# Kernel optimization log

Hardware: AMD Instinct MI355X
Metric: run time of the kernel (lower is better)

The kernel has to match this reference:

```python
import jax, jax.numpy as jnp
import numpy as np

N = 40000            # atoms
ER = 2_500_000       # radial edges
EA = 1_200_000       # angular edges
P = 4_000_000        # angle triples
NUM_SPECIES = 4      # H,C,N,O
CUTOFF = 5.2
ANG_CUTOFF = 3.5
RADIAL_ETA = 16.0
ANGULAR_ETA = 8.0
RDIV = 16
ADIV = 4
ZETA = 32.0
ASEC = 4
RSTART = 0.8
ASTART = 0.8


def setup_inputs() -> dict:
    key = jax.random.key(0)
    ks = jax.random.split(key, 12)
    species = jax.random.randint(ks[0], (N,), 0, NUM_SPECIES, dtype=jnp.int32)
    rad_distances = jax.random.uniform(ks[1], (ER,), jnp.float32, RSTART, CUTOFF)
    rad_switch = jax.random.uniform(ks[2], (ER,), jnp.float32)
    edge_src = jax.random.randint(ks[3], (ER,), 0, N, dtype=jnp.int32)
    edge_dst = jax.random.randint(ks[4], (ER,), 0, N, dtype=jnp.int32)
    ang_distances = jax.random.uniform(ks[5], (EA,), jnp.float32, ASTART, ANG_CUTOFF)
    ang_switch = jax.random.uniform(ks[6], (EA,), jnp.float32)
    angles = jax.random.uniform(ks[7], (P,), jnp.float32, 0.0, float(np.pi))
    central_atom = jax.random.randint(ks[8], (P,), 0, N, dtype=jnp.int32)
    angle_src = jax.random.randint(ks[9], (P,), 0, EA, dtype=jnp.int32)
    angle_dst = jax.random.randint(ks[10], (P,), 0, EA, dtype=jnp.int32)
    ang_edge_dst = jax.random.randint(ks[11], (EA,), 0, N, dtype=jnp.int32)
    return {
        "species": species,
        "rad_distances": rad_distances,
        "rad_switch": rad_switch,
        "edge_src": edge_src,
        "edge_dst": edge_dst,
        "ang_distances": ang_distances,
        "ang_switch": ang_switch,
        "angles": angles,
        "central_atom": central_atom,
        "angle_src": angle_src,
        "angle_dst": angle_dst,
        "ang_edge_dst": ang_edge_dst,
    }


def _triu_table(nsp):
    s1, s2 = np.triu_indices(nsp, 0)
    t = np.zeros((nsp, nsp), dtype=np.int32)
    t[s1, s2] = np.arange(s1.shape[0], dtype=np.int32)
    t[s2, s1] = t[s1, s2]
    return jnp.asarray(t)


def reference(species, rad_distances, rad_switch, edge_src, edge_dst,
              ang_distances, ang_switch, angles, central_atom,
              angle_src, angle_dst, ang_edge_dst):
    n_atoms = species.shape[0]
    nsp = NUM_SPECIES
    nsp_pair = nsp * (nsp + 1) // 2
    indices = species  # already species-order indices in [0, nsp)

    # ---- radial AEV ----
    shiftR = jnp.asarray(-np.linspace(RSTART, CUTOFF, RDIV + 1)[None, :-1],
                         dtype=rad_distances.dtype)  # [1, RDIV]
    x2 = RADIAL_ETA * (rad_distances[:, None] + shiftR) ** 2       # [ER, RDIV]
    radial_terms = jnp.exp(-x2) * (0.25 * rad_switch)[:, None]
    radial_index = edge_src * nsp + indices[edge_dst]
    radial_aev = jax.ops.segment_sum(radial_terms, radial_index,
                                     num_segments=nsp * n_atoms)
    radial_aev = radial_aev.reshape(n_atoms, nsp * RDIV)

    # ---- angular AEV ----
    dist = 0.5 * ANGULAR_ETA ** 0.5 * ang_distances                # [EA]
    d12 = (dist[angle_src] + dist[angle_dst])[:, None]             # [P, 1]
    angle_start = np.pi / (2 * ASEC)
    shiftZ = jnp.asarray(-(np.linspace(0, np.pi, ASEC + 1) + angle_start)[None, :-1],
                         dtype=dist.dtype)                          # [1, ASEC]
    shiftA = jnp.asarray(-ANGULAR_ETA ** 0.5 *
                         np.linspace(ASTART, ANG_CUTOFF, ADIV + 1)[None, :-1],
                         dtype=dist.dtype)                          # [1, ADIV]
    sw = ang_switch * (2.0 * 0.5 ** ZETA) ** 0.5                   # [EA]
    f1 = sw[angle_src] * sw[angle_dst]                             # [P]
    factor1 = f1[:, None] * (1 + jnp.cos(angles[:, None] + shiftZ)) ** ZETA  # [P, ASEC]
    factor2 = jnp.exp(-(d12 + shiftA) ** 2)                        # [P, ADIV]
    angular_terms = (factor1[:, None, :] * factor2[:, :, None]).reshape(-1, ASEC * ADIV)

    idx_dest = indices[ang_edge_dst]                               # [EA]
    triu = _triu_table(nsp)
    angular_index = central_atom * nsp_pair + triu[idx_dest[angle_src], idx_dest[angle_dst]]
    angular_aev = jax.ops.segment_sum(angular_terms, angular_index,
                                      num_segments=nsp_pair * n_atoms)
    angular_aev = angular_aev.reshape(n_atoms, nsp_pair * ASEC * ADIV)

    return jnp.concatenate((radial_aev, angular_aev), axis=-1)     # [N, 224]
```

## Files before the change

### kernel.cpp

```cpp
#include <hip/hip_runtime.h>


constexpr int kOutCols  = 224;
constexpr int kAngBase  = 64;
constexpr int kABUCK    = 64;
constexpr int kMaxBins  = 640;
constexpr int kSCap     = 4096;
constexpr int kNBR      = 640;
constexpr int kNBA      = 1024;
constexpr int kRCap     = 4608;
constexpr int kACap     = 7168;
constexpr int kRC       = 12;
constexpr int kCapR     = 16;
constexpr int kCapA     = 12;
constexpr int kOvf      = 512;

__device__ __constant__ int c_triu[16] = {0,1,2,3, 1,4,5,6, 2,5,7,8, 3,6,8,9};
__device__ __constant__ float c_ca[4] = {0.92387953f, 0.38268343f, -0.38268343f, -0.92387953f};
__device__ __constant__ float c_sa[4] = {0.38268343f, 0.92387953f,  0.92387953f,  0.38268343f};
__device__ __constant__ float c_sh[4] = {-2.2627417f, -4.1719303f, -6.0811183f, -7.9903066f};

constexpr float kThQ  = 20860.437f;
constexpr float kRevD = 7.6295109e-6f;
constexpr float kD12B = 2.2627417f;
constexpr float kD12S = 1.4974026e-2f;
constexpr float kF1D  = 1.1732081e-13f;
constexpr float kRdS  = 930.6818f;
constexpr float kRdD  = 1.0744811e-3f;
constexpr float kRswD = 6.1050061e-5f;

__device__ __forceinline__ int scan1024_exc(int cv, int tid, int* wsum, int* total)
{
    int lane = tid & 63, wv = tid >> 6;
    int x = cv;
    #pragma unroll
    for (int o = 1; o < 64; o <<= 1) {
        int t = __shfl_up(x, o, 64);
        if (lane >= o) x += t;
    }
    if (lane == 63) wsum[wv] = x;
    __syncthreads();
    if (wv == 0 && lane < 16) {
        int s = wsum[lane];
        #pragma unroll
        for (int o = 1; o < 16; o <<= 1) {
            int t = __shfl_up(s, o, 64);
            if (lane >= o) s += t;
        }
        wsum[lane] = s;
    }
    __syncthreads();
    int base = (wv == 0) ? 0 : wsum[wv - 1];
    *total = wsum[15];
    return base + x - cv;
}

__global__ void prep(const float* __restrict__ ang_d, const float* __restrict__ ang_sw,
                     const int* __restrict__ aed, const int* __restrict__ species,
                     unsigned short* __restrict__ eaq, int EA)
{
    int i = blockIdx.x * blockDim.x + threadIdx.x;
    if (i >= EA) return;
    float dq = fmaxf(ang_d[i] - 0.8f, 0.0f) * (255.0f / 2.7f);
    unsigned qd = min((unsigned)(dq + 0.5f), 255u);
    unsigned qs = min((unsigned)(fmaxf(ang_sw[i], 0.0f) * 63.0f + 0.5f), 63u);
    unsigned sp = (unsigned)species[aed[i]];
    eaq[i] = (unsigned short)(qd | (qs << 8) | (sp << 14));
}

__global__ __launch_bounds__(1024)
void scat(const float* __restrict__ rd, const float* __restrict__ rsw,
          const int* __restrict__ esrc, const int* __restrict__ edst,
          const int* __restrict__ species,
          unsigned* __restrict__ rrec, int* __restrict__ offRT, int ER, int chR,
          const float* __restrict__ angles, const int* __restrict__ cat,
          const int* __restrict__ asrc, const int* __restrict__ adst,
          const unsigned short* __restrict__ eaq,
          uint2* __restrict__ arec, int* __restrict__ offAT, int P, int chA)
{
    __shared__ uint2 sbuf[kMaxBins * kCapA];
    __shared__ int cur[kMaxBins], off[kMaxBins + 1];
    __shared__ int wsum[16];
    __shared__ int ovfn;
    __shared__ uint4 ovfb[kOvf];
    int tid = threadIdx.x;

    if (blockIdx.x < kNBR) {
        unsigned* stage = (unsigned*)sbuf;
        for (int t = tid; t < kMaxBins; t += 1024) cur[t] = t * kCapR;
        if (tid == 0) ovfn = 0;
        __syncthreads();
        int sb  = blockIdx.x;
        int beg = sb * chR, end = min(beg + chR, ER);
        int i0 = beg + tid * 4;
        if (i0 < end) {
            float4 d4 = *reinterpret_cast<const float4*>(rd + i0);
            float4 s4 = *reinterpret_cast<const float4*>(rsw + i0);
            int4   e4 = *reinterpret_cast<const int4*>(esrc + i0);
            int4   t4 = *reinterpret_cast<const int4*>(edst + i0);
            unsigned sa = (unsigned)species[t4.x], sb2 = (unsigned)species[t4.y];
            unsigned sc2 = (unsigned)species[t4.z], sd = (unsigned)species[t4.w];
            auto bld = [](float d, float s, int e, unsigned sp, unsigned& v, int& k) {
                unsigned qd = min((unsigned)(fmaxf(d - 0.8f, 0.0f) * kRdS + 0.5f), 4095u);
                unsigned qs = min((unsigned)(fmaxf(s, 0.0f) * 4095.0f + 0.5f), 4095u);
                v = qd | (qs << 12) | (sp << 24) | ((unsigned)(e & 63) << 26);
                k = e >> 6;
            };
            unsigned v0, v1, v2, v3; int k0, k1, k2, k3;
            bld(d4.x, s4.x, e4.x, sa,  v0, k0);
            bld(d4.y, s4.y, e4.y, sb2, v1, k1);
            bld(d4.z, s4.z, e4.z, sc2, v2, k2);
            bld(d4.w, s4.w, e4.w, sd,  v3, k3);
            auto ins = [&](int k, unsigned v) {
                int pos = atomicAdd(&cur[k], 1);
                int loc = pos - k * kCapR;
                if (loc < kCapR) stage[pos] = v;
                else {
                    int o = atomicAdd(&ovfn, 1);
                    if (o < kOvf) { ovfb[o].x = (unsigned)k; ovfb[o].y = (unsigned)loc; ovfb[o].z = v; }
                }
            };
            ins(k0, v0); ins(k1, v1); ins(k2, v2); ins(k3, v3);
        }
        __syncthreads();
        int cv = (tid < kMaxBins) ? (cur[tid] - tid * kCapR) : 0;
        int tot;
        int exc = scan1024_exc(cv, tid, wsum, &tot);
        if (tid < kMaxBins) off[tid] = exc;
        if (tid == 0) off[kMaxBins] = tot;
        if (tid < kMaxBins) cur[tid] = min(cv, kCapR);
        __syncthreads();
        for (int s = tid; s < kMaxBins * kCapR; s += 1024) {
            int bin = s >> 4, loc = s & (kCapR - 1);
            if (loc < cur[bin]) rrec[beg + off[bin] + loc] = stage[s];
        }
        int no = min(ovfn, kOvf);
        for (int o = tid; o < no; o += 1024) {
            uint4 e = ovfb[o];
            rrec[beg + off[e.x] + (int)e.y] = e.z;
        }
        for (int t = tid; t <= kMaxBins; t += 1024) offRT[t * kNBR + sb] = off[t];
    } else {
        for (int t = tid; t < kMaxBins; t += 1024) cur[t] = t * kCapA;
        if (tid == 0) ovfn = 0;
        __syncthreads();
        int sb  = blockIdx.x - kNBR;
        int beg = sb * chA, end = min(beg + chA, P);
        int i0 = beg + tid * 4;
        if (i0 < end) {
            uint4  s4 = *reinterpret_cast<const uint4*>(asrc + i0);
            uint4  d4 = *reinterpret_cast<const uint4*>(adst + i0);
            float4 t4 = *reinterpret_cast<const float4*>(angles + i0);
            int4   c4 = *reinterpret_cast<const int4*>(cat + i0);
            unsigned qa0 = eaq[s4.x], qb0 = eaq[d4.x];
            unsigned qa1 = eaq[s4.y], qb1 = eaq[d4.y];
            unsigned qa2 = eaq[s4.z], qb2 = eaq[d4.z];
            unsigned qa3 = eaq[s4.w], qb3 = eaq[d4.w];
            auto bld = [](unsigned qa, unsigned qb, float th, int atom, uint2& rv, int& key) {
                unsigned qd12 = (qa & 255u) + (qb & 255u);
                unsigned qf1  = ((qa >> 8) & 63u) * ((qb >> 8) & 63u);
                int pair = c_triu[(qa >> 14) * 4 + (qb >> 14)];
                unsigned qt = min((unsigned)(fmaxf(th, 0.0f) * kThQ + 0.5f), 65535u);
                rv.x = qt | (qd12 << 16);
                rv.y = qf1 | ((unsigned)((atom & 63) * 10 + pair) << 16);
                key = atom >> 6;
            };
            uint2 r0, r1, r2, r3; int k0, k1, k2, k3;
            bld(qa0, qb0, t4.x, c4.x, r0, k0);
            bld(qa1, qb1, t4.y, c4.y, r1, k1);
            bld(qa2, qb2, t4.z, c4.z, r2, k2);
            bld(qa3, qb3, t4.w, c4.w, r3, k3);
            auto ins = [&](int k, uint2 r) {
                int pos = atomicAdd(&cur[k], 1);
                int loc = pos - k * kCapA;
                if (loc < kCapA) sbuf[pos] = r;
                else {
                    int o = atomicAdd(&ovfn, 1);
                    if (o < kOvf) { ovfb[o].x = (unsigned)k; ovfb[o].y = (unsigned)loc; ovfb[o].z = r.x; ovfb[o].w = r.y; }
                }
            };
            ins(k0, r0); ins(k1, r1); ins(k2, r2); ins(k3, r3);
        }
        __syncthreads();
        int cv = (tid < kMaxBins) ? (cur[tid] - tid * kCapA) : 0;
        int tot;
        int exc = scan1024_exc(cv, tid, wsum, &tot);
        if (tid < kMaxBins) off[tid] = exc;
        if (tid == 0) off[kMaxBins] = tot;
        if (tid < kMaxBins) cur[tid] = min(cv, kCapA);
        __syncthreads();
        for (int s = tid; s < kMaxBins * kCapA; s += 1024) {
            int bin = s / kCapA, loc = s - bin * kCapA;
            if (loc < cur[bin]) arec[beg + off[bin] + loc] = sbuf[s];
        }
        int no = min(ovfn, kOvf);
        for (int o = tid; o < no; o += 1024) {
            uint4 e = ovfb[o];
            uint2 r; r.x = e.z; r.y = e.w;
            arec[beg + off[e.x] + (int)e.y] = r;
        }
        for (int t = tid; t <= kMaxBins; t += 1024) offAT[t * kNBA + sb] = off[t];
    }
}

__global__ __launch_bounds__(1024)
void acc_rad(const unsigned* __restrict__ rrec, const int* __restrict__ offRT,
             int chR, float* __restrict__ out, int N)
{
    __shared__ unsigned rb[kRCap];
    __shared__ int cnt[64], off[65], cur[64];
    int b = blockIdx.x, tid = threadIdx.x;
    int gstart = 0, glen = 0;
    if (tid < kNBR) {
        int s0 = offRT[b * kNBR + tid];
        int s1 = offRT[(b + 1) * kNBR + tid];
        gstart = tid * chR + s0;
        glen   = s1 - s0;
    }
    unsigned rr[kRC];
    int gl = min(glen, kRC);
    #pragma unroll
    for (int q = 0; q < kRC; ++q) if (q < gl) rr[q] = rrec[gstart + q];
    if (tid < 64) cnt[tid] = 0;
    __syncthreads();
    #pragma unroll
    for (int q = 0; q < kRC; ++q) if (q < gl) atomicAdd(&cnt[(rr[q] >> 26) & 63], 1);
    for (int p = gstart + kRC; p < gstart + glen; ++p)
        atomicAdd(&cnt[(rrec[p] >> 26) & 63], 1);
    __syncthreads();
    if (tid < 64) {
        int x = cnt[tid], v = x;
        #pragma unroll
        for (int o = 1; o < 64; o <<= 1) {
            int t = __shfl_up(v, o, 64);
            if (tid >= o) v += t;
        }
        off[tid] = v - x; cur[tid] = v - x;
        if (tid == 63) off[64] = v;
    }
    __syncthreads();
    #pragma unroll
    for (int q = 0; q < kRC; ++q)
        if (q < gl) {
            int pos = atomicAdd(&cur[(rr[q] >> 26) & 63], 1);
            if (pos < kRCap) rb[pos] = rr[q];
        }
    for (int p = gstart + kRC; p < gstart + glen; ++p) {
        unsigned r = rrec[p];
        int pos = atomicAdd(&cur[(r >> 26) & 63], 1);
        if (pos < kRCap) rb[pos] = r;
    }
    __syncthreads();
    int lane = tid & 63, wave = tid >> 6;
    int q = lane >> 4, k = lane & 15;
    float ck = fmaf(0.275f, (float)k, 0.8f);
    for (int row = wave; row < kABUCK; row += 16) {
        int s  = min(off[row], kRCap);
        int e1 = min(off[row + 1], kRCap);
        float a0 = 0, a1 = 0, a2 = 0, a3 = 0;
        for (int p = s + q; p < e1; p += 4) {
            unsigned r = rb[p];
            float d  = fmaf((float)(r & 4095u), kRdD, 0.8f);
            float sw = (float)((r >> 12) & 4095u) * kRswD;
            int sp   = (r >> 24) & 3;
            float x  = d - ck;
            float v  = sw * __expf(-16.0f * x * x);
            a0 += (sp == 0) ? v : 0.0f;
            a1 += (sp == 1) ? v : 0.0f;
            a2 += (sp == 2) ? v : 0.0f;
            a3 += (sp == 3) ? v : 0.0f;
        }
        a0 += __shfl_xor(a0, 16, 64); a0 += __shfl_xor(a0, 32, 64);
        a1 += __shfl_xor(a1, 16, 64); a1 += __shfl_xor(a1, 32, 64);
        a2 += __shfl_xor(a2, 16, 64); a2 += __shfl_xor(a2, 32, 64);
        a3 += __shfl_xor(a3, 16, 64); a3 += __shfl_xor(a3, 32, 64);
        float val = (q == 0) ? a0 : (q == 1) ? a1 : (q == 2) ? a2 : a3;
        int atom = b * kABUCK + row;
        if (atom < N) out[(size_t)atom * kOutCols + lane] = val;
    }
}

__global__ __launch_bounds__(1024)
void acc_ang(const uint2* __restrict__ arec, const int* __restrict__ offAT,
             int chA, float* __restrict__ out, int N)
{
    __shared__ uint2 ab[kACap];
    __shared__ int cnt[640], off[641], cur[640];
    __shared__ int wsum[16];
    int b = blockIdx.x, tid = threadIdx.x;
    int s0 = offAT[b * kNBA + tid];
    int s1 = offAT[(b + 1) * kNBA + tid];
    int gstart = tid * chA + s0;
    int glen   = s1 - s0;
    uint2 rr[kRC];
    int gl = min(glen, kRC);
    #pragma unroll
    for (int q = 0; q < kRC; ++q) if (q < gl) rr[q] = arec[gstart + q];
    for (int t = tid; t < 640; t += 1024) cnt[t] = 0;
    __syncthreads();
    #pragma unroll
    for (int q = 0; q < kRC; ++q) if (q < gl) atomicAdd(&cnt[rr[q].y >> 16], 1);
    for (int p = gstart + kRC; p < gstart + glen; ++p)
        atomicAdd(&cnt[arec[p].y >> 16], 1);
    __syncthreads();
    int cv = (tid < 640) ? cnt[tid] : 0;
    int tot;
    int exc = scan1024_exc(cv, tid, wsum, &tot);
    if (tid < 640) { off[tid] = exc; cur[tid] = exc; }
    if (tid == 0) off[640] = tot;
    __syncthreads();
    #pragma unroll
    for (int q = 0; q < kRC; ++q)
        if (q < gl) {
            int pos = atomicAdd(&cur[rr[q].y >> 16], 1);
            if (pos < kACap) ab[pos] = rr[q];
        }
    for (int p = gstart + kRC; p < gstart + glen; ++p) {
        uint2 r = arec[p];
        int pos = atomicAdd(&cur[r.y >> 16], 1);
        if (pos < kACap) ab[pos] = r;
    }
    __syncthreads();
    int g = tid >> 4, lam = tid & 15;
    int q = lam >> 2, j = lam & 3;
    float caj = c_ca[j], saj = c_sa[j];
    int atom = b * kABUCK + g;
    if (atom < N) {
        float* orow = out + (size_t)atom * kOutCols + kAngBase;
        for (int pr = 0; pr < 10; ++pr) {
            int s  = min(off[g * 10 + pr], kACap);
            int e1 = min(off[g * 10 + pr + 1], kACap);
            float s0v = 0, s1v = 0, s2v = 0, s3v = 0;
            for (int p = s + q; p < e1; p += 4) {
                uint2 r = ab[p];
                float rev = (float)(r.x & 0xFFFFu) * kRevD;
                float d12 = fmaf((float)(r.x >> 16), kD12S, kD12B);
                float f1  = (float)(r.y & 0xFFFFu) * kF1D;
                float sn, cs;
                asm("v_sin_f32 %0, %1" : "=v"(sn) : "v"(rev));
                asm("v_cos_f32 %0, %1" : "=v"(cs) : "v"(rev));
                float cj = fmaf(cs, caj, sn * saj);
                float t  = 1.0f + cj;
                float t2 = t * t, t4 = t2 * t2, t8 = t4 * t4, t16 = t8 * t8;
                float w  = f1 * (t16 * t16);
                float x0 = d12 + c_sh[0]; s0v = fmaf(w, __expf(-x0 * x0), s0v);
                float x1 = d12 + c_sh[1]; s1v = fmaf(w, __expf(-x1 * x1), s1v);
                float x2 = d12 + c_sh[2]; s2v = fmaf(w, __expf(-x2 * x2), s2v);
                float x3 = d12 + c_sh[3]; s3v = fmaf(w, __expf(-x3 * x3), s3v);
            }
            s0v += __shfl_xor(s0v, 4, 64); s0v += __shfl_xor(s0v, 8, 64);
            s1v += __shfl_xor(s1v, 4, 64); s1v += __shfl_xor(s1v, 8, 64);
            s2v += __shfl_xor(s2v, 4, 64); s2v += __shfl_xor(s2v, 8, 64);
            s3v += __shfl_xor(s3v, 4, 64); s3v += __shfl_xor(s3v, 8, 64);
            float val = (q == 0) ? s0v : (q == 1) ? s1v : (q == 2) ? s2v : s3v;
            orow[pr * 16 + lam] = val;
        }
    }
}

__global__ void radial_kernel(const float* __restrict__ rd, const float* __restrict__ rsw,
                              const int* __restrict__ esrc, const int* __restrict__ edst,
                              const int* __restrict__ species,
                              float* __restrict__ out, int ER)
{
    int i = blockIdx.x * blockDim.x + threadIdx.x;
    if (i >= ER) return;
    float d   = rd[i];
    float sw  = 0.25f * rsw[i];
    int   src = esrc[i];
    int   sp  = species[edst[i]];
    float* base = out + (size_t)src * kOutCols + sp * 16;
    float t = (d - 0.8f) * (1.0f / 0.275f);
    int klo = max(0, (int)ceilf(t - 4.0f));
    int khi = min(15, (int)floorf(t + 4.0f));
    for (int k = klo; k <= khi; ++k) {
        float x = d - fmaf(0.275f, (float)k, 0.8f);
        float v = sw * __expf(-16.0f * x * x);
        if (v > 1e-8f) unsafeAtomicAdd(base + k, v);
    }
}

__global__ void angular_fallback(const float* __restrict__ angles, const int* __restrict__ cat,
                                 const int* __restrict__ asrc, const int* __restrict__ adst,
                                 const float* __restrict__ ang_d, const float* __restrict__ ang_sw,
                                 const int* __restrict__ aed, const int* __restrict__ species,
                                 float* __restrict__ out, int P)
{
    int i = blockIdx.x * blockDim.x + threadIdx.x;
    if (i >= P) return;
    int e1i = asrc[i], e2i = adst[i];
    float d1 = 1.41421356237f * ang_d[e1i];
    float d2 = 1.41421356237f * ang_d[e2i];
    float w1 = 2.1579187e-05f * ang_sw[e1i];
    float w2 = 2.1579187e-05f * ang_sw[e2i];
    int sp1 = species[aed[e1i]], sp2 = species[aed[e2i]];
    float d12 = d1 + d2;
    float f1  = w1 * w2;
    int pair = c_triu[sp1 * 4 + sp2];
    float* base = out + (size_t)cat[i] * kOutCols + kAngBase + pair * 16;

    float s, c;
    __sincosf(angles[i], &s, &c);
    const float ca0 = 0.92387953f, sa0 = 0.38268343f;
    float cth[4];
    cth[0] = fmaf(c,  ca0, s * sa0);
    cth[1] = fmaf(c,  sa0, s * ca0);
    cth[2] = fmaf(c, -sa0, s * ca0);
    cth[3] = fmaf(c, -ca0, s * sa0);
    float fac1[4];
    #pragma unroll
    for (int j = 0; j < 4; ++j) {
        float t  = 1.0f + cth[j];
        float t2 = t * t, t4 = t2 * t2, t8 = t4 * t4, t16 = t8 * t8;
        fac1[j]  = f1 * (t16 * t16);
    }
    const float shiftA[4] = {-2.2627417f, -4.1719303f, -6.0811183f, -7.9903066f};
    #pragma unroll
    for (int ii = 0; ii < 4; ++ii) {
        float x  = d12 + shiftA[ii];
        float f2 = __expf(-x * x);
        if (f2 < 1e-7f) continue;
        #pragma unroll
        for (int j = 0; j < 4; ++j) {
            float v = f2 * fac1[j];
            if (v > 1e-8f) unsafeAtomicAdd(base + ii * 4 + j, v);
        }
    }
}

extern "C" void kernel_launch(void* const* d_in, const int* in_sizes, int n_in,
                              void* d_out, int out_size, void* d_ws, size_t ws_size,
                              hipStream_t stream)
{
    const int*   species = (const int*)  d_in[0];
    const float* rad_d   = (const float*)d_in[1];
    const float* rad_sw  = (const float*)d_in[2];
    const int*   esrc    = (const int*)  d_in[3];
    const int*   edst    = (const int*)  d_in[4];
    const float* ang_d   = (const float*)d_in[5];
    const float* ang_sw  = (const float*)d_in[6];
    const float* angles  = (const float*)d_in[7];
    const int*   cat     = (const int*)  d_in[8];
    const int*   asrc    = (const int*)  d_in[9];
    const int*   adst    = (const int*)  d_in[10];
    const int*   aed     = (const int*)  d_in[11];
    float* out = (float*)d_out;

    const int N  = in_sizes[0];
    const int ER = in_sizes[1];
    const int EA = in_sizes[5];
    const int P  = in_sizes[7];

    const int NB  = (N + kABUCK - 1) / kABUCK;
    const int chR = (((ER + kNBR - 1) / kNBR) + 3) & ~3;
    const int chA = (((P  + kNBA - 1) / kNBA) + 3) & ~3;

    char* w = (char*)d_ws;
    size_t pos = 0;
    auto take = [&](size_t nbytes) {
        size_t cur = pos;
        pos = (pos + nbytes + 255) & ~(size_t)255;
        return cur;
    };
    size_t ea_o   = take((size_t)EA * 2);
    size_t rrec_o = take((size_t)kNBR * chR * 4);
    size_t arec_o = take((size_t)kNBA * chA * 8);
    size_t ort_o  = take((size_t)(kMaxBins + 1) * kNBR * 4);
    size_t oat_o  = take((size_t)(kMaxBins + 1) * kNBA * 4);
    const size_t need = pos;

    const bool sorted_ok = (ws_size >= need) && (NB <= kMaxBins) &&
                           (chR <= kSCap) && (chA <= kSCap) &&
                           ((P & 3) == 0) && ((ER & 3) == 0);

    if (sorted_ok) {
        unsigned short* eaq = (unsigned short*)(w + ea_o);
        unsigned* rrec  = (unsigned*)(w + rrec_o);
        uint2*    arec  = (uint2*)(w + arec_o);
        int*      offRT = (int*)(w + ort_o);
        int*      offAT = (int*)(w + oat_o);

        prep<<<(EA + 255) / 256, 256, 0, stream>>>(ang_d, ang_sw, aed, species, eaq, EA);
        scat<<<kNBR + kNBA, 1024, 0, stream>>>(rad_d, rad_sw, esrc, edst, species,
                                               rrec, offRT, ER, chR,
                                               angles, cat, asrc, adst, eaq,
                                               arec, offAT, P, chA);
        acc_rad<<<NB, 1024, 0, stream>>>(rrec, offRT, chR, out, N);
        acc_ang<<<NB, 1024, 0, stream>>>(arec, offAT, chA, out, N);
    } else {
        hipMemsetAsync(d_out, 0, (size_t)out_size * sizeof(float), stream);
        radial_kernel<<<(ER + 255) / 256, 256, 0, stream>>>(rad_d, rad_sw, esrc, edst, species, out, ER);
        angular_fallback<<<(P + 255) / 256, 256, 0, stream>>>(angles, cat, asrc, adst,
                                                              ang_d, ang_sw, aed, species, out, P);
    }
}
```

Baseline: 178.7 us.

## Regroup stages into fused launches to overlap radial scatter with angular prep

Moves the angular-edge quantisation (prep) into the same launch as the radial scatter, and moves the radial accumulation into the same launch as the angular scatter, using block-index ranges to select each role. This cuts four launches to three and lets independent stages run side by side on the GPU, so idle tails between dependent kernels are reduced. Shared memory is now carved manually from one raw buffer per role. The fused1 kernel now needs only the radial staging buffer, which may lower its LDS footprint. The cost is that fused2 blocks reserve the larger angular LDS size even when doing radial accumulation, which may limit occupancy.

```diff
diff --git a/kernel.cpp b/kernel.cpp
--- a/kernel.cpp
+++ b/kernel.cpp
@@ -55,30 +55,15 @@
     return base + x - cv;
 }
 
-__global__ void prep(const float* __restrict__ ang_d, const float* __restrict__ ang_sw,
-                     const int* __restrict__ aed, const int* __restrict__ species,
-                     unsigned short* __restrict__ eaq, int EA)
-{
-    int i = blockIdx.x * blockDim.x + threadIdx.x;
-    if (i >= EA) return;
-    float dq = fmaxf(ang_d[i] - 0.8f, 0.0f) * (255.0f / 2.7f);
-    unsigned qd = min((unsigned)(dq + 0.5f), 255u);
-    unsigned qs = min((unsigned)(fmaxf(ang_sw[i], 0.0f) * 63.0f + 0.5f), 63u);
-    unsigned sp = (unsigned)species[aed[i]];
-    eaq[i] = (unsigned short)(qd | (qs << 8) | (sp << 14));
-}
-
 __global__ __launch_bounds__(1024)
-void scat(const float* __restrict__ rd, const float* __restrict__ rsw,
-          const int* __restrict__ esrc, const int* __restrict__ edst,
-          const int* __restrict__ species,
-          unsigned* __restrict__ rrec, int* __restrict__ offRT, int ER, int chR,
-          const float* __restrict__ angles, const int* __restrict__ cat,
-          const int* __restrict__ asrc, const int* __restrict__ adst,
-          const unsigned short* __restrict__ eaq,
-          uint2* __restrict__ arec, int* __restrict__ offAT, int P, int chA)
-{
-    __shared__ uint2 sbuf[kMaxBins * kCapA];
+void fused1(const float* __restrict__ rd, const float* __restrict__ rsw,
+            const int* __restrict__ esrc, const int* __restrict__ edst,
+            const int* __restrict__ species,
+            unsigned* __restrict__ rrec, int* __restrict__ offRT, int ER, int chR,
+            const float* __restrict__ ang_d, const float* __restrict__ ang_sw,
+            const int* __restrict__ aed, unsigned short* __restrict__ eaq, int EA)
+{
+    __shared__ unsigned stage[kMaxBins * kCapR];
     __shared__ int cur[kMaxBins], off[kMaxBins + 1];
     __shared__ int wsum[16];
     __shared__ int ovfn;
@@ -86,7 +71,6 @@
     int tid = threadIdx.x;
 
     if (blockIdx.x < kNBR) {
-        unsigned* stage = (unsigned*)sbuf;
         for (int t = tid; t < kMaxBins; t += 1024) cur[t] = t * kCapR;
         if (tid == 0) ovfn = 0;
         __syncthreads();
@@ -141,10 +125,40 @@
         }
         for (int t = tid; t <= kMaxBins; t += 1024) offRT[t * kNBR + sb] = off[t];
     } else {
+        int i = (blockIdx.x - kNBR) * 1024 + tid;
+        if (i < EA) {
+            float dq = fmaxf(ang_d[i] - 0.8f, 0.0f) * (255.0f / 2.7f);
+            unsigned qd = min((unsigned)(dq + 0.5f), 255u);
+            unsigned qs = min((unsigned)(fmaxf(ang_sw[i], 0.0f) * 63.0f + 0.5f), 63u);
+            unsigned sp = (unsigned)species[aed[i]];
+            eaq[i] = (unsigned short)(qd | (qs << 8) | (sp << 14));
+        }
+    }
+}
+
+__global__ __launch_bounds__(1024)
+void fused2(const float* __restrict__ angles, const int* __restrict__ cat,
+            const int* __restrict__ asrc, const int* __restrict__ adst,
+            const unsigned short* __restrict__ eaq,
+            uint2* __restrict__ arec, int* __restrict__ offAT, int P, int chA,
+            const unsigned* __restrict__ rrec, const int* __restrict__ offRT,
+            int chR, float* __restrict__ out, int N)
+{
+    __shared__ uint4 raw[4680];
+    int tid = threadIdx.x;
+
+    if (blockIdx.x < kNBA) {
+        uint2* sbuf = (uint2*)raw;
+        int*   cur  = (int*)((char*)raw + 61440);
+        int*   off  = (int*)((char*)raw + 64000);
+        int*   wsum = (int*)((char*)raw + 66564);
+        int*   ovfn = (int*)((char*)raw + 66628);
+        uint4* ovfb = (uint4*)((char*)raw + 66640);
+
         for (int t = tid; t < kMaxBins; t += 1024) cur[t] = t * kCapA;
-        if (tid == 0) ovfn = 0;
-        __syncthreads();
-        int sb  = blockIdx.x - kNBR;
+        if (tid == 0) *ovfn = 0;
+        __syncthreads();
+        int sb  = blockIdx.x;
         int beg = sb * chA, end = min(beg + chA, P);
         int i0 = beg + tid * 4;
         if (i0 < end) {
@@ -175,7 +189,7 @@
                 int loc = pos - k * kCapA;
                 if (loc < kCapA) sbuf[pos] = r;
                 else {
-                    int o = atomicAdd(&ovfn, 1);
+                    int o = atomicAdd(ovfn, 1);
                     if (o < kOvf) { ovfb[o].x = (unsigned)k; ovfb[o].y = (unsigned)loc; ovfb[o].z = r.x; ovfb[o].w = r.y; }
                 }
             };
@@ -193,90 +207,88 @@
             int bin = s / kCapA, loc = s - bin * kCapA;
             if (loc < cur[bin]) arec[beg + off[bin] + loc] = sbuf[s];
         }
-        int no = min(ovfn, kOvf);
+        int no = min(*ovfn, kOvf);
         for (int o = tid; o < no; o += 1024) {
             uint4 e = ovfb[o];
             uint2 r; r.x = e.z; r.y = e.w;
             arec[beg + off[e.x] + (int)e.y] = r;
         }
         for (int t = tid; t <= kMaxBins; t += 1024) offAT[t * kNBA + sb] = off[t];
-    }
-}
-
-__global__ __launch_bounds__(1024)
-void acc_rad(const unsigned* __restrict__ rrec, const int* __restrict__ offRT,
-             int chR, float* __restrict__ out, int N)
-{
-    __shared__ unsigned rb[kRCap];
-    __shared__ int cnt[64], off[65], cur[64];
-    int b = blockIdx.x, tid = threadIdx.x;
-    int gstart = 0, glen = 0;
-    if (tid < kNBR) {
-        int s0 = offRT[b * kNBR + tid];
-        int s1 = offRT[(b + 1) * kNBR + tid];
-        gstart = tid * chR + s0;
-        glen   = s1 - s0;
-    }
-    unsigned rr[kRC];
-    int gl = min(glen, kRC);
-    #pragma unroll
-    for (int q = 0; q < kRC; ++q) if (q < gl) rr[q] = rrec[gstart + q];
-    if (tid < 64) cnt[tid] = 0;
-    __syncthreads();
-    #pragma unroll
-    for (int q = 0; q < kRC; ++q) if (q < gl) atomicAdd(&cnt[(rr[q] >> 26) & 63], 1);
-    for (int p = gstart + kRC; p < gstart + glen; ++p)
-        atomicAdd(&cnt[(rrec[p] >> 26) & 63], 1);
-    __syncthreads();
-    if (tid < 64) {
-        int x = cnt[tid], v = x;
+    } else {
+        unsigned* rb  = (unsigned*)raw;
+        int*      cnt = (int*)((char*)raw + 18432);
+        int*      off = (int*)((char*)raw + 18688);
+        int*      cur = (int*)((char*)raw + 18948);
+
+        int b = blockIdx.x - kNBA;
+        int gstart = 0, glen = 0;
+        if (tid < kNBR) {
+            int s0 = offRT[b * kNBR + tid];
+            int s1 = offRT[(b + 1) * kNBR + tid];
+            gstart = tid * chR + s0;
+            glen   = s1 - s0;
+        }
+        unsigned rr[kRC];
+        int gl = min(glen, kRC);
         #pragma unroll
-        for (int o = 1; o < 64; o <<= 1) {
-            int t = __shfl_up(v, o, 64);
-            if (tid >= o) v += t;
-        }
-        off[tid] = v - x; cur[tid] = v - x;
-        if (tid == 63) off[64] = v;
-    }
-    __syncthreads();
-    #pragma unroll
-    for (int q = 0; q < kRC; ++q)
-        if (q < gl) {
-            int pos = atomicAdd(&cur[(rr[q] >> 26) & 63], 1);
-            if (pos < kRCap) rb[pos] = rr[q];
-        }
-    for (int p = gstart + kRC; p < gstart + glen; ++p) {
-        unsigned r = rrec[p];
-        int pos = atomicAdd(&cur[(r >> 26) & 63], 1);
-        if (pos < kRCap) rb[pos] = r;
-    }
-    __syncthreads();
-    int lane = tid & 63, wave = tid >> 6;
-    int q = lane >> 4, k = lane & 15;
-    float ck = fmaf(0.275f, (float)k, 0.8f);
-    for (int row = wave; row < kABUCK; row += 16) {
-        int s  = min(off[row], kRCap);
-        int e1 = min(off[row + 1], kRCap);
-        float a0 = 0, a1 = 0, a2 = 0, a3 = 0;
-        for (int p = s + q; p < e1; p += 4) {
-            unsigned r = rb[p];
-            float d  = fmaf((float)(r & 4095u), kRdD, 0.8f);
-            float sw = (float)((r >> 12) & 4095u) * kRswD;
-            int sp   = (r >> 24) & 3;
-            float x  = d - ck;
-            float v  = sw * __expf(-16.0f * x * x);
-            a0 += (sp == 0) ? v : 0.0f;
-            a1 += (sp == 1) ? v : 0.0f;
-            a2 += (sp == 2) ? v : 0.0f;
-            a3 += (sp == 3) ? v : 0.0f;
-        }
-        a0 += __shfl_xor(a0, 16, 64); a0 += __shfl_xor(a0, 32, 64);
-        a1 += __shfl_xor(a1, 16, 64); a1 += __shfl_xor(a1, 32, 64);
-        a2 += __shfl_xor(a2, 16, 64); a2 += __shfl_xor(a2, 32, 64);
-        a3 += __shfl_xor(a3, 16, 64); a3 += __shfl_xor(a3, 32, 64);
-        float val = (q == 0) ? a0 : (q == 1) ? a1 : (q == 2) ? a2 : a3;
-        int atom = b * kABUCK + row;
-        if (atom < N) out[(size_t)atom * kOutCols + lane] = val;
+        for (int q = 0; q < kRC; ++q) if (q < gl) rr[q] = rrec[gstart + q];
+        if (tid < 64) cnt[tid] = 0;
+        __syncthreads();
+        #pragma unroll
+        for (int q = 0; q < kRC; ++q) if (q < gl) atomicAdd(&cnt[(rr[q] >> 26) & 63], 1);
+        for (int p = gstart + kRC; p < gstart + glen; ++p)
+            atomicAdd(&cnt[(rrec[p] >> 26) & 63], 1);
+        __syncthreads();
+        if (tid < 64) {
+            int x = cnt[tid], v = x;
+            #pragma unroll
+            for (int o = 1; o < 64; o <<= 1) {
+                int t = __shfl_up(v, o, 64);
+                if (tid >= o) v += t;
+            }
+            off[tid] = v - x; cur[tid] = v - x;
+            if (tid == 63) off[64] = v;
+        }
+        __syncthreads();
+        #pragma unroll
+        for (int q = 0; q < kRC; ++q)
+            if (q < gl) {
+                int pos = atomicAdd(&cur[(rr[q] >> 26) & 63], 1);
+                if (pos < kRCap) rb[pos] = rr[q];
+            }
+        for (int p = gstart + kRC; p < gstart + glen; ++p) {
+            unsigned r = rrec[p];
+            int pos = atomicAdd(&cur[(r >> 26) & 63], 1);
+            if (pos < kRCap) rb[pos] = r;
+        }
+        __syncthreads();
+        int lane = tid & 63, wave = tid >> 6;
+        int q = lane >> 4, k = lane & 15;
+        float ck = fmaf(0.275f, (float)k, 0.8f);
+        for (int row = wave; row < kABUCK; row += 16) {
+            int s  = min(off[row], kRCap);
+            int e1 = min(off[row + 1], kRCap);
+            float a0 = 0, a1 = 0, a2 = 0, a3 = 0;
+            for (int p = s + q; p < e1; p += 4) {
+                unsigned r = rb[p];
+                float d  = fmaf((float)(r & 4095u), kRdD, 0.8f);
+                float sw = (float)((r >> 12) & 4095u) * kRswD;
+                int sp   = (r >> 24) & 3;
+                float x  = d - ck;
+                float v  = sw * __expf(-16.0f * x * x);
+                a0 += (sp == 0) ? v : 0.0f;
+                a1 += (sp == 1) ? v : 0.0f;
+                a2 += (sp == 2) ? v : 0.0f;
+                a3 += (sp == 3) ? v : 0.0f;
+            }
+            a0 += __shfl_xor(a0, 16, 64); a0 += __shfl_xor(a0, 32, 64);
+            a1 += __shfl_xor(a1, 16, 64); a1 += __shfl_xor(a1, 32, 64);
+            a2 += __shfl_xor(a2, 16, 64); a2 += __shfl_xor(a2, 32, 64);
+            a3 += __shfl_xor(a3, 16, 64); a3 += __shfl_xor(a3, 32, 64);
+            float val = (q == 0) ? a0 : (q == 1) ? a1 : (q == 2) ? a2 : a3;
+            int atom = b * kABUCK + row;
+            if (atom < N) out[(size_t)atom * kOutCols + lane] = val;
+        }
     }
 }
 
@@ -454,6 +466,7 @@
     const int NB  = (N + kABUCK - 1) / kABUCK;
     const int chR = (((ER + kNBR - 1) / kNBR) + 3) & ~3;
     const int chA = (((P  + kNBA - 1) / kNBA) + 3) & ~3;
+    const int prepB = (EA + 1023) / 1024;
 
     char* w = (char*)d_ws;
     size_t pos = 0;
@@ -480,12 +493,12 @@
         int*      offRT = (int*)(w + ort_o);
         int*      offAT = (int*)(w + oat_o);
 
-        prep<<<(EA + 255) / 256, 256, 0, stream>>>(ang_d, ang_sw, aed, species, eaq, EA);
-        scat<<<kNBR + kNBA, 1024, 0, stream>>>(rad_d, rad_sw, esrc, edst, species,
-                                               rrec, offRT, ER, chR,
-                                               angles, cat, asrc, adst, eaq,
-                                               arec, offAT, P, chA);
-        acc_rad<<<NB, 1024, 0, stream>>>(rrec, offRT, chR, out, N);
+        fused1<<<kNBR + prepB, 1024, 0, stream>>>(rad_d, rad_sw, esrc, edst, species,
+                                                  rrec, offRT, ER, chR,
+                                                  ang_d, ang_sw, aed, eaq, EA);
+        fused2<<<kNBA + NB, 1024, 0, stream>>>(angles, cat, asrc, adst, eaq,
+                                               arec, offAT, P, chA,
+                                               rrec, offRT, chR, out, N);
         acc_ang<<<NB, 1024, 0, stream>>>(arec, offAT, chA, out, N);
     } else {
         hipMemsetAsync(d_out, 0, (size_t)out_size * sizeof(float), stream);
```

New measurement: 172.8 us (median of 2 runs). -3.3%, faster.
